# Kernel optimization log

Measured on AMD Instinct MI355X. Metric: run time of the kernel, lower is better.

## Reference

```python
import jax, jax.numpy as jnp
import numpy as np

DT = 0.01
DT_SCALE = 1.0

B, D, R = 4096, 1024, 256

def setup_inputs() -> dict:
    key = jax.random.key(0)
    kx, kv, kf, ku, kw = jax.random.split(key, 5)
    x = jax.random.normal(kx, (B, D), dtype=jnp.float32)
    v = jax.random.normal(kv, (B, D), dtype=jnp.float32)
    force = jax.random.normal(kf, (B, D), dtype=jnp.float32)
    # low-rank Christoffel factors; scaled down so the quadratic term stays stable
    U = jax.random.normal(ku, (D, R), dtype=jnp.float32) * (1.0 / np.sqrt(D))
    W = jax.random.normal(kw, (R, D), dtype=jnp.float32) * (1.0 / np.sqrt(R))
    return {"x": x, "v": v, "force": force, "U": U, "W": W, "steps": 8}

def christoffel(v, U, W):
    # Gamma(v, v) = ((v @ U) ** 2) @ W  -- factored quadratic form
    p = v @ U            # [B, R]
    return (p * p) @ W   # [B, D]

def reference(x, v, force, U, W, steps):
    dt = DT * DT_SCALE

    def step(carry, _):
        cx, cv = carry
        acc = force - christoffel(cv, U, W)
        cx = cx + dt * cv
        cv = cv + dt * acc
        return (cx, cv), None

    (cx, cv), _ = jax.lax.scan(step, (x, v), None, length=steps)
    return (cx, cv)
```

## Files before the change

kernel.cpp:

```cpp
#include <hip/hip_runtime.h>
#include <hip/hip_bf16.h>


#define BB 4096
#define DD 1024
#define RR 256
#define DT 0.01f

typedef __attribute__((ext_vector_type(8))) short short8;
typedef __attribute__((ext_vector_type(4))) float floatx4;

static __device__ inline unsigned short f2bf(float f) {
    union { float f; unsigned int u; } c; c.f = f;
    unsigned int u = c.u;
    u += 0x7fffu + ((u >> 16) & 1u);
    return (unsigned short)(u >> 16);
}

__global__ void pack_kernel(const float* __restrict__ U, const float* __restrict__ W,
                            short* __restrict__ Up, short* __restrict__ Wp) {
    int t = blockIdx.x * blockDim.x + threadIdx.x;
    if (t < 32768) {
        int lane = t & 63;
        int nl = lane & 15, kq = lane >> 4;
        int idx = t >> 6;
        int nt = idx & 15, kt = idx >> 4;
        short8 o;
#pragma unroll
        for (int j = 0; j < 8; j++) {
            int k = kt * 32 + kq * 8 + j;
            int n = nt * 16 + nl;
            o[j] = (short)f2bf(U[k * RR + n]);
        }
        ((short8*)Up)[t] = o;
    } else {
        int t2 = t - 32768;
        int lane = t2 & 63;
        int nl = lane & 15, kq = lane >> 4;
        int idx = t2 >> 6;
        int nt = idx & 63, kt = idx >> 6;
        short8 o;
#pragma unroll
        for (int j = 0; j < 8; j++) {
            int k = kt * 32 + kq * 8 + j;
            int n = nt * 16 + nl;
            o[j] = (short)f2bf(W[k * DD + n]);
        }
        ((short8*)Wp)[t2] = o;
    }
}

__global__ __launch_bounds__(1024, 4)
void euler_kernel(const float* __restrict__ x0,
                  const float* __restrict__ v0,
                  const float* __restrict__ force,
                  const short8* __restrict__ Up,
                  const short8* __restrict__ Wp,
                  const int* __restrict__ steps_p,
                  float* __restrict__ out) {
    __shared__ __align__(16) short v_lds[16][1032];
    __shared__ __align__(16) short p2_lds[16][264];

    const int tid  = threadIdx.x;
    const int wave = tid >> 6;
    const int lane = tid & 63;
    const int nl   = lane & 15;
    const int quad = lane >> 4;
    const int row0 = blockIdx.x * 16;

    const int steps = steps_p[0];

    float v_reg[4][4], f_reg[4][4], sv[4][4];

#pragma unroll
    for (int t = 0; t < 4; t++) {
        int col = 64 * wave + 16 * t + nl;
#pragma unroll
        for (int r = 0; r < 4; r++) {
            int row = 4 * quad + r;
            long g = (long)(row0 + row) * DD + col;
            v_reg[t][r] = v0[g];
            f_reg[t][r] = force[g];
            sv[t][r] = 0.0f;
            v_lds[row][col] = (short)f2bf(v_reg[t][r]);
        }
    }
    __syncthreads();

    for (int s = 0; s < steps; s++) {
        floatx4 acc1 = {0.f, 0.f, 0.f, 0.f};
#pragma unroll 4
        for (int kt = 0; kt < 32; kt++) {
            short8 a = *(const short8*)&v_lds[nl][kt * 32 + quad * 8];
            short8 b = Up[(kt * 16 + wave) * 64 + lane];
            acc1 = __builtin_amdgcn_mfma_f32_16x16x32_bf16(a, b, acc1, 0, 0, 0);
        }
#pragma unroll
        for (int r = 0; r < 4; r++) {
            float p = acc1[r];
            p2_lds[4 * quad + r][16 * wave + nl] = (short)f2bf(p * p);
        }
        __syncthreads();

        floatx4 acc[4];
#pragma unroll
        for (int t = 0; t < 4; t++) acc[t] = (floatx4){0.f, 0.f, 0.f, 0.f};
#pragma unroll 2
        for (int kt = 0; kt < 8; kt++) {
            short8 a = *(const short8*)&p2_lds[nl][kt * 32 + quad * 8];
#pragma unroll
            for (int t = 0; t < 4; t++) {
                short8 b = Wp[(kt * 64 + 4 * wave + t) * 64 + lane];
                acc[t] = __builtin_amdgcn_mfma_f32_16x16x32_bf16(a, b, acc[t], 0, 0, 0);
            }
        }
#pragma unroll
        for (int t = 0; t < 4; t++) {
            int col = 64 * wave + 16 * t + nl;
#pragma unroll
            for (int r = 0; r < 4; r++) {
                int row = 4 * quad + r;
                float gma = acc[t][r];
                sv[t][r] += v_reg[t][r];
                v_reg[t][r] += DT * (f_reg[t][r] - gma);
                v_lds[row][col] = (short)f2bf(v_reg[t][r]);
            }
        }
        __syncthreads();
    }

    float (*stage)[1032] = reinterpret_cast<float(*)[1032]>(&v_lds[0][0]);
    const float4* x4 = reinterpret_cast<const float4*>(x0);
    float4* out4 = reinterpret_cast<float4*>(out);

    for (int sel = 0; sel < 2; sel++) {
        for (int half = 0; half < 2; half++) {
            __syncthreads();
            if ((quad >> 1) == half) {
#pragma unroll
                for (int t = 0; t < 4; t++) {
                    int col = 64 * wave + 16 * t + nl;
#pragma unroll
                    for (int r = 0; r < 4; r++) {
                        int lrow = (4 * quad + r) & 7;
                        stage[lrow][col] = sel ? v_reg[t][r] : DT * sv[t][r];
                    }
                }
            }
            __syncthreads();
            for (int i = tid; i < 2048; i += 1024) {
                int lrow = i >> 8;
                int c4 = i & 255;
                long gi = (long)(row0 + half * 8 + lrow) * 256 + c4;
                float4 val = *(const float4*)&stage[lrow][c4 * 4];
                if (sel == 0) {
                    float4 xv = x4[gi];
                    val.x += xv.x; val.y += xv.y; val.z += xv.z; val.w += xv.w;
                    out4[gi] = val;
                } else {
                    out4[(long)BB * 256 + gi] = val;
                }
            }
        }
    }
}

extern "C" void kernel_launch(void* const* d_in, const int* in_sizes, int n_in,
                              void* d_out, int out_size, void* d_ws, size_t ws_size,
                              hipStream_t stream) {
    const float* x     = (const float*)d_in[0];
    const float* v     = (const float*)d_in[1];
    const float* force = (const float*)d_in[2];
    const float* U     = (const float*)d_in[3];
    const float* W     = (const float*)d_in[4];
    const int*   steps = (const int*)d_in[5];

    short* Up = (short*)d_ws;
    short* Wp = Up + 32768 * 8;

    pack_kernel<<<256, 256, 0, stream>>>(U, W, Up, Wp);
    euler_kernel<<<256, 1024, 0, stream>>>(x, v, force,
                                           (const short8*)Up, (const short8*)Wp,
                                           steps, (float*)d_out);
}
```

Baseline: 180.2 us.

## Process 32 rows per block to reuse weight fragments, pack force/sum in fp16

Each block now handles 32 batch rows instead of 16, so every Up/Wp fragment loaded from global memory feeds two MFMAs, halving weight traffic per row. To fit the doubled per-thread state in registers, force and the running velocity sum are stored as packed fp16 pairs. The pack kernel is rewritten to read U/W with coalesced float4 loads and scatter the bf16 outputs. The grid shrinks to 128 blocks, which leaves fewer blocks than the MI355X's 256 CUs and cuts parallelism. The fp16 accumulation of the velocity sum also costs some accuracy.

```diff
diff --git a/kernel.cpp b/kernel.cpp
--- a/kernel.cpp
+++ b/kernel.cpp
@@ -1,5 +1,6 @@
 #include <hip/hip_runtime.h>
 #include <hip/hip_bf16.h>
+#include <hip/hip_fp16.h>
 
 
 #define BB 4096
@@ -17,40 +18,49 @@
     return (unsigned short)(u >> 16);
 }
 
-__global__ void pack_kernel(const float* __restrict__ U, const float* __restrict__ W,
-                            short* __restrict__ Up, short* __restrict__ Wp) {
+static __device__ inline unsigned int pk2h(float a, float b) {
+    unsigned int ha = __half_as_ushort(__float2half_rn(a));
+    unsigned int hb = __half_as_ushort(__float2half_rn(b));
+    return ha | (hb << 16);
+}
+static __device__ inline float lo_h(unsigned int u) {
+    return __half2float(__ushort_as_half((unsigned short)(u & 0xFFFFu)));
+}
+static __device__ inline float hi_h(unsigned int u) {
+    return __half2float(__ushort_as_half((unsigned short)(u >> 16)));
+}
+
+__global__ __launch_bounds__(256)
+void pack_kernel(const float* __restrict__ U, const float* __restrict__ W,
+                 short* __restrict__ Up, short* __restrict__ Wp) {
     int t = blockIdx.x * blockDim.x + threadIdx.x;
-    if (t < 32768) {
-        int lane = t & 63;
-        int nl = lane & 15, kq = lane >> 4;
-        int idx = t >> 6;
-        int nt = idx & 15, kt = idx >> 4;
-        short8 o;
-#pragma unroll
-        for (int j = 0; j < 8; j++) {
-            int k = kt * 32 + kq * 8 + j;
-            int n = nt * 16 + nl;
-            o[j] = (short)f2bf(U[k * RR + n]);
-        }
-        ((short8*)Up)[t] = o;
+    if (t < 65536) {
+        int k = t >> 6, n4 = t & 63;
+        float4 u = *(const float4*)&U[k * RR + 4 * n4];
+        int kt = k >> 5, kq = (k >> 3) & 3, j = k & 7;
+        float uv[4] = {u.x, u.y, u.z, u.w};
+#pragma unroll
+        for (int i = 0; i < 4; i++) {
+            int n = 4 * n4 + i;
+            int nt = n >> 4, nl = n & 15;
+            Up[(((kt * 16 + nt) * 64) + kq * 16 + nl) * 8 + j] = (short)f2bf(uv[i]);
+        }
     } else {
-        int t2 = t - 32768;
-        int lane = t2 & 63;
-        int nl = lane & 15, kq = lane >> 4;
-        int idx = t2 >> 6;
-        int nt = idx & 63, kt = idx >> 6;
-        short8 o;
-#pragma unroll
-        for (int j = 0; j < 8; j++) {
-            int k = kt * 32 + kq * 8 + j;
-            int n = nt * 16 + nl;
-            o[j] = (short)f2bf(W[k * DD + n]);
-        }
-        ((short8*)Wp)[t2] = o;
-    }
-}
-
-__global__ __launch_bounds__(1024, 4)
+        int t2 = t - 65536;
+        int k = t2 >> 8, n4 = t2 & 255;
+        float4 w = *(const float4*)&W[k * DD + 4 * n4];
+        int kt = k >> 5, kq = (k >> 3) & 3, j = k & 7;
+        float wv[4] = {w.x, w.y, w.z, w.w};
+#pragma unroll
+        for (int i = 0; i < 4; i++) {
+            int n = 4 * n4 + i;
+            int nt = n >> 4, nl = n & 15;
+            Wp[(((kt * 64 + nt) * 64) + kq * 16 + nl) * 8 + j] = (short)f2bf(wv[i]);
+        }
+    }
+}
+
+__global__ __launch_bounds__(1024)
 void euler_kernel(const float* __restrict__ x0,
                   const float* __restrict__ v0,
                   const float* __restrict__ force,
@@ -58,72 +68,101 @@
                   const short8* __restrict__ Wp,
                   const int* __restrict__ steps_p,
                   float* __restrict__ out) {
-    __shared__ __align__(16) short v_lds[16][1032];
-    __shared__ __align__(16) short p2_lds[16][264];
+    __shared__ __align__(16) short v_lds[32][1032];
+    __shared__ __align__(16) short p2_lds[32][264];
 
     const int tid  = threadIdx.x;
     const int wave = tid >> 6;
     const int lane = tid & 63;
     const int nl   = lane & 15;
     const int quad = lane >> 4;
-    const int row0 = blockIdx.x * 16;
+    const int row0 = blockIdx.x * 32;
 
     const int steps = steps_p[0];
 
-    float v_reg[4][4], f_reg[4][4], sv[4][4];
-
-#pragma unroll
-    for (int t = 0; t < 4; t++) {
-        int col = 64 * wave + 16 * t + nl;
-#pragma unroll
-        for (int r = 0; r < 4; r++) {
-            int row = 4 * quad + r;
-            long g = (long)(row0 + row) * DD + col;
-            v_reg[t][r] = v0[g];
-            f_reg[t][r] = force[g];
-            sv[t][r] = 0.0f;
-            v_lds[row][col] = (short)f2bf(v_reg[t][r]);
+    float v_reg[2][4][4];
+    unsigned int sv_pk[2][4][2];
+    unsigned int f_pk[2][4][2];
+
+#pragma unroll
+    for (int rg = 0; rg < 2; rg++) {
+#pragma unroll
+        for (int t = 0; t < 4; t++) {
+            int col = 64 * wave + 16 * t + nl;
+            float fv[4];
+#pragma unroll
+            for (int r = 0; r < 4; r++) {
+                int row = 16 * rg + 4 * quad + r;
+                long g = (long)(row0 + row) * DD + col;
+                v_reg[rg][t][r] = v0[g];
+                fv[r] = force[g];
+                v_lds[row][col] = (short)f2bf(v_reg[rg][t][r]);
+            }
+            f_pk[rg][t][0] = pk2h(fv[0], fv[1]);
+            f_pk[rg][t][1] = pk2h(fv[2], fv[3]);
+            sv_pk[rg][t][0] = 0u;
+            sv_pk[rg][t][1] = 0u;
         }
     }
     __syncthreads();
 
     for (int s = 0; s < steps; s++) {
+        floatx4 acc0 = {0.f, 0.f, 0.f, 0.f};
         floatx4 acc1 = {0.f, 0.f, 0.f, 0.f};
 #pragma unroll 4
         for (int kt = 0; kt < 32; kt++) {
-            short8 a = *(const short8*)&v_lds[nl][kt * 32 + quad * 8];
-            short8 b = Up[(kt * 16 + wave) * 64 + lane];
-            acc1 = __builtin_amdgcn_mfma_f32_16x16x32_bf16(a, b, acc1, 0, 0, 0);
+            short8 a0 = *(const short8*)&v_lds[nl][kt * 32 + quad * 8];
+            short8 a1 = *(const short8*)&v_lds[16 + nl][kt * 32 + quad * 8];
+            short8 b  = Up[(kt * 16 + wave) * 64 + lane];
+            acc0 = __builtin_amdgcn_mfma_f32_16x16x32_bf16(a0, b, acc0, 0, 0, 0);
+            acc1 = __builtin_amdgcn_mfma_f32_16x16x32_bf16(a1, b, acc1, 0, 0, 0);
         }
 #pragma unroll
         for (int r = 0; r < 4; r++) {
-            float p = acc1[r];
-            p2_lds[4 * quad + r][16 * wave + nl] = (short)f2bf(p * p);
+            float p0 = acc0[r], p1 = acc1[r];
+            p2_lds[4 * quad + r][16 * wave + nl]      = (short)f2bf(p0 * p0);
+            p2_lds[16 + 4 * quad + r][16 * wave + nl] = (short)f2bf(p1 * p1);
         }
         __syncthreads();
 
-        floatx4 acc[4];
-#pragma unroll
-        for (int t = 0; t < 4; t++) acc[t] = (floatx4){0.f, 0.f, 0.f, 0.f};
+        floatx4 acc[2][4];
+#pragma unroll
+        for (int rg = 0; rg < 2; rg++)
+#pragma unroll
+            for (int t = 0; t < 4; t++) acc[rg][t] = (floatx4){0.f, 0.f, 0.f, 0.f};
 #pragma unroll 2
         for (int kt = 0; kt < 8; kt++) {
-            short8 a = *(const short8*)&p2_lds[nl][kt * 32 + quad * 8];
+            short8 a0 = *(const short8*)&p2_lds[nl][kt * 32 + quad * 8];
+            short8 a1 = *(const short8*)&p2_lds[16 + nl][kt * 32 + quad * 8];
 #pragma unroll
             for (int t = 0; t < 4; t++) {
                 short8 b = Wp[(kt * 64 + 4 * wave + t) * 64 + lane];
-                acc[t] = __builtin_amdgcn_mfma_f32_16x16x32_bf16(a, b, acc[t], 0, 0, 0);
-            }
-        }
-#pragma unroll
-        for (int t = 0; t < 4; t++) {
-            int col = 64 * wave + 16 * t + nl;
-#pragma unroll
-            for (int r = 0; r < 4; r++) {
-                int row = 4 * quad + r;
-                float gma = acc[t][r];
-                sv[t][r] += v_reg[t][r];
-                v_reg[t][r] += DT * (f_reg[t][r] - gma);
-                v_lds[row][col] = (short)f2bf(v_reg[t][r]);
+                acc[0][t] = __builtin_amdgcn_mfma_f32_16x16x32_bf16(a0, b, acc[0][t], 0, 0, 0);
+                acc[1][t] = __builtin_amdgcn_mfma_f32_16x16x32_bf16(a1, b, acc[1][t], 0, 0, 0);
+            }
+        }
+#pragma unroll
+        for (int rg = 0; rg < 2; rg++) {
+#pragma unroll
+            for (int t = 0; t < 4; t++) {
+                int col = 64 * wave + 16 * t + nl;
+                int rowb = 16 * rg + 4 * quad;
+#pragma unroll
+                for (int p = 0; p < 2; p++) {
+                    float f0 = lo_h(f_pk[rg][t][p]), f1 = hi_h(f_pk[rg][t][p]);
+                    float s0 = lo_h(sv_pk[rg][t][p]), s1 = hi_h(sv_pk[rg][t][p]);
+                    float vv0 = v_reg[rg][t][2 * p];
+                    float vv1 = v_reg[rg][t][2 * p + 1];
+                    s0 += vv0;
+                    s1 += vv1;
+                    vv0 += DT * (f0 - acc[rg][t][2 * p]);
+                    vv1 += DT * (f1 - acc[rg][t][2 * p + 1]);
+                    sv_pk[rg][t][p] = pk2h(s0, s1);
+                    v_reg[rg][t][2 * p]     = vv0;
+                    v_reg[rg][t][2 * p + 1] = vv1;
+                    v_lds[rowb + 2 * p][col]     = (short)f2bf(vv0);
+                    v_lds[rowb + 2 * p + 1][col] = (short)f2bf(vv1);
+                }
             }
         }
         __syncthreads();
@@ -133,17 +172,28 @@
     const float4* x4 = reinterpret_cast<const float4*>(x0);
     float4* out4 = reinterpret_cast<float4*>(out);
 
+#pragma unroll
     for (int sel = 0; sel < 2; sel++) {
-        for (int half = 0; half < 2; half++) {
+#pragma unroll
+        for (int chunk = 0; chunk < 4; chunk++) {
+            const int crg = chunk >> 1;
+            const int ch  = chunk & 1;
             __syncthreads();
-            if ((quad >> 1) == half) {
+            if ((quad >> 1) == ch) {
 #pragma unroll
                 for (int t = 0; t < 4; t++) {
                     int col = 64 * wave + 16 * t + nl;
 #pragma unroll
                     for (int r = 0; r < 4; r++) {
-                        int lrow = (4 * quad + r) & 7;
-                        stage[lrow][col] = sel ? v_reg[t][r] : DT * sv[t][r];
+                        float val;
+                        if (sel) {
+                            val = v_reg[crg][t][r];
+                        } else {
+                            unsigned int u = sv_pk[crg][t][r >> 1];
+                            float sva = (r & 1) ? hi_h(u) : lo_h(u);
+                            val = DT * sva;
+                        }
+                        stage[(4 * quad + r) & 7][col] = val;
                     }
                 }
             }
@@ -151,7 +201,7 @@
             for (int i = tid; i < 2048; i += 1024) {
                 int lrow = i >> 8;
                 int c4 = i & 255;
-                long gi = (long)(row0 + half * 8 + lrow) * 256 + c4;
+                long gi = (long)(row0 + chunk * 8 + lrow) * 256 + c4;
                 float4 val = *(const float4*)&stage[lrow][c4 * 4];
                 if (sel == 0) {
                     float4 xv = x4[gi];
@@ -178,8 +228,8 @@
     short* Up = (short*)d_ws;
     short* Wp = Up + 32768 * 8;
 
-    pack_kernel<<<256, 256, 0, stream>>>(U, W, Up, Wp);
-    euler_kernel<<<256, 1024, 0, stream>>>(x, v, force,
+    pack_kernel<<<512, 256, 0, stream>>>(U, W, Up, Wp);
+    euler_kernel<<<128, 1024, 0, stream>>>(x, v, force,
                                            (const short8*)Up, (const short8*)Wp,
                                            steps, (float*)d_out);
 }
```

Result: slower. 214.4 us (+19.0%).

## Software-pipeline U/W fragment loads with register queues, stagger per-wave k-start

Applied to the files above, without the earlier changes.

The main kernel now prefetches the bf16 B fragments of U and W into 8-deep register queues ahead of each MFMA, so global/L2 load latency overlaps matrix work. It issues the W loads before the p^2 barrier and the next step's U loads after the second GEMM. Each wave starts its k-loop at a different offset to spread L2/LDS traffic. Barriers are replaced with a lighter LDS-only waitcnt plus s_barrier, and the pack kernel reads U/W with coalesced float4 loads using twice as many threads. The cost is higher register pressure, and occupancy is already tight at 1024-thread blocks.

```diff
diff --git a/kernel.cpp b/kernel.cpp
--- a/kernel.cpp
+++ b/kernel.cpp
@@ -17,36 +17,39 @@
     return (unsigned short)(u >> 16);
 }
 
-__global__ void pack_kernel(const float* __restrict__ U, const float* __restrict__ W,
-                            short* __restrict__ Up, short* __restrict__ Wp) {
+static __device__ inline void lds_barrier() {
+    asm volatile("s_waitcnt lgkmcnt(0)" ::: "memory");
+    __builtin_amdgcn_s_barrier();
+    asm volatile("" ::: "memory");
+}
+
+__global__ __launch_bounds__(256)
+void pack_kernel(const float* __restrict__ U, const float* __restrict__ W,
+                 short* __restrict__ Up, short* __restrict__ Wp) {
     int t = blockIdx.x * blockDim.x + threadIdx.x;
-    if (t < 32768) {
-        int lane = t & 63;
-        int nl = lane & 15, kq = lane >> 4;
-        int idx = t >> 6;
-        int nt = idx & 15, kt = idx >> 4;
-        short8 o;
-#pragma unroll
-        for (int j = 0; j < 8; j++) {
-            int k = kt * 32 + kq * 8 + j;
-            int n = nt * 16 + nl;
-            o[j] = (short)f2bf(U[k * RR + n]);
-        }
-        ((short8*)Up)[t] = o;
+    if (t < 65536) {
+        int k = t >> 6, n4 = t & 63;
+        float4 u = *(const float4*)&U[k * RR + 4 * n4];
+        int kt = k >> 5, kq = (k >> 3) & 3, j = k & 7;
+        float uv[4] = {u.x, u.y, u.z, u.w};
+#pragma unroll
+        for (int i = 0; i < 4; i++) {
+            int n = 4 * n4 + i;
+            int nt = n >> 4, nl = n & 15;
+            Up[(((kt * 16 + nt) * 64) + kq * 16 + nl) * 8 + j] = (short)f2bf(uv[i]);
+        }
     } else {
-        int t2 = t - 32768;
-        int lane = t2 & 63;
-        int nl = lane & 15, kq = lane >> 4;
-        int idx = t2 >> 6;
-        int nt = idx & 63, kt = idx >> 6;
-        short8 o;
-#pragma unroll
-        for (int j = 0; j < 8; j++) {
-            int k = kt * 32 + kq * 8 + j;
-            int n = nt * 16 + nl;
-            o[j] = (short)f2bf(W[k * DD + n]);
-        }
-        ((short8*)Wp)[t2] = o;
+        int t2 = t - 65536;
+        int k = t2 >> 8, n4 = t2 & 255;
+        float4 w = *(const float4*)&W[k * DD + 4 * n4];
+        int kt = k >> 5, kq = (k >> 3) & 3, j = k & 7;
+        float wv[4] = {w.x, w.y, w.z, w.w};
+#pragma unroll
+        for (int i = 0; i < 4; i++) {
+            int n = 4 * n4 + i;
+            int nt = n >> 4, nl = n & 15;
+            Wp[(((kt * 64 + nt) * 64) + kq * 16 + nl) * 8 + j] = (short)f2bf(wv[i]);
+        }
     }
 }
 
@@ -70,6 +73,9 @@
 
     const int steps = steps_p[0];
 
+    const int kt0  = (2 * wave) & 31;
+    const int kt0b = wave & 7;
+
     float v_reg[4][4], f_reg[4][4], sv[4][4];
 
 #pragma unroll
@@ -85,35 +91,63 @@
             v_lds[row][col] = (short)f2bf(v_reg[t][r]);
         }
     }
-    __syncthreads();
+
+    short8 bq[8];
+#pragma unroll
+    for (int i = 0; i < 8; i++)
+        bq[i] = Up[(((kt0 + i) & 31) * 16 + wave) * 64 + lane];
+
+    lds_barrier();
 
     for (int s = 0; s < steps; s++) {
         floatx4 acc1 = {0.f, 0.f, 0.f, 0.f};
-#pragma unroll 4
-        for (int kt = 0; kt < 32; kt++) {
+#pragma unroll
+        for (int kk = 0; kk < 32; kk++) {
+            int kt = (kt0 + kk) & 31;
             short8 a = *(const short8*)&v_lds[nl][kt * 32 + quad * 8];
-            short8 b = Up[(kt * 16 + wave) * 64 + lane];
+            short8 b = bq[kk & 7];
+            if (kk < 24)
+                bq[kk & 7] = Up[(((kt0 + kk + 8) & 31) * 16 + wave) * 64 + lane];
             acc1 = __builtin_amdgcn_mfma_f32_16x16x32_bf16(a, b, acc1, 0, 0, 0);
         }
+
+        short8 wq[8];
+#pragma unroll
+        for (int i = 0; i < 8; i++) {
+            int kt = (kt0b + (i >> 2)) & 7;
+            wq[i] = Wp[(kt * 64 + 4 * wave + (i & 3)) * 64 + lane];
+        }
+
 #pragma unroll
         for (int r = 0; r < 4; r++) {
             float p = acc1[r];
             p2_lds[4 * quad + r][16 * wave + nl] = (short)f2bf(p * p);
         }
-        __syncthreads();
+        lds_barrier();
 
         floatx4 acc[4];
 #pragma unroll
         for (int t = 0; t < 4; t++) acc[t] = (floatx4){0.f, 0.f, 0.f, 0.f};
-#pragma unroll 2
-        for (int kt = 0; kt < 8; kt++) {
+#pragma unroll
+        for (int kk = 0; kk < 8; kk++) {
+            int kt = (kt0b + kk) & 7;
             short8 a = *(const short8*)&p2_lds[nl][kt * 32 + quad * 8];
 #pragma unroll
             for (int t = 0; t < 4; t++) {
-                short8 b = Wp[(kt * 64 + 4 * wave + t) * 64 + lane];
+                int m = 4 * kk + t;
+                short8 b = wq[m & 7];
+                if (m < 24) {
+                    int ktn = (kt0b + kk + 2) & 7;
+                    wq[m & 7] = Wp[(ktn * 64 + 4 * wave + t) * 64 + lane];
+                }
                 acc[t] = __builtin_amdgcn_mfma_f32_16x16x32_bf16(a, b, acc[t], 0, 0, 0);
             }
         }
+
+#pragma unroll
+        for (int i = 0; i < 8; i++)
+            bq[i] = Up[(((kt0 + i) & 31) * 16 + wave) * 64 + lane];
+
 #pragma unroll
         for (int t = 0; t < 4; t++) {
             int col = 64 * wave + 16 * t + nl;
@@ -126,7 +160,7 @@
                 v_lds[row][col] = (short)f2bf(v_reg[t][r]);
             }
         }
-        __syncthreads();
+        lds_barrier();
     }
 
     float (*stage)[1032] = reinterpret_cast<float(*)[1032]>(&v_lds[0][0]);
@@ -178,7 +212,7 @@
     short* Up = (short*)d_ws;
     short* Wp = Up + 32768 * 8;
 
-    pack_kernel<<<256, 256, 0, stream>>>(U, W, Up, Wp);
+    pack_kernel<<<512, 256, 0, stream>>>(U, W, Up, Wp);
     euler_kernel<<<256, 1024, 0, stream>>>(x, v, force,
                                            (const short8*)Up, (const short8*)Wp,
                                            steps, (float*)d_out);
```

New measurement: 392.4 us. +117.7%, slower.
